# Performance work log

Measured on AMD Instinct MI355X. Metric: run time of the kernel, lower is better.

## Reference

```python
import jax, jax.numpy as jnp
import numpy as np

NC = 120000            # active coarse voxels
D, H, W = 16, 256, 256 # coarse grid
NF = 2 * NC            # active fine voxels (upsample output)
CIN, COUT = 128, 64


def _build_pairs():
    """Build spconv-style (in_idx, out_idx) pair maps per kernel offset.
    Padding: in_idx = NC (dummy zero feature row), out_idx = n_out (dropped row)."""
    rng = np.random.default_rng(0)
    flat = rng.choice(D * H * W, size=NC, replace=False)
    cz, cy, cx = np.unravel_index(flat, (D, H, W))
    lut = np.full(D * H * W, -1, np.int64)
    lut[flat] = np.arange(NC)

    def subm(offs):
        P = np.full((len(offs), NC, 2), NC, np.int32)
        for k, (dz, dy, dx) in enumerate(offs):
            nz, ny, nx = cz + dz, cy + dy, cx + dx
            ok = (nz >= 0) & (nz < D) & (ny >= 0) & (ny < H) & (nx >= 0) & (nx < W)
            nb = np.full(NC, -1, np.int64)
            nb[ok] = lut[(nz[ok] * H + ny[ok]) * W + nx[ok]]
            ok &= nb >= 0
            idx = np.nonzero(ok)[0]
            P[k, :len(idx), 0] = nb[idx]
            P[k, :len(idx), 1] = idx
        return P

    o33 = [(a, b, c) for a in (-1, 0, 1) for b in (-1, 0, 1) for c in (-1, 0, 1)]
    o13 = [(0, b, c) for b in (-1, 0, 1) for c in (-1, 0, 1)]   # kernel (1,3,3)
    o31 = [(a, 0, c) for a in (-1, 0, 1) for c in (-1, 0, 1)]   # kernel (3,1,3)

    # fine coords: each coarse voxel c spawns fine voxels 2c and 2c+1 (all dims)
    fz = np.concatenate([cz * 2, cz * 2 + 1])
    fy = np.concatenate([cy * 2, cy * 2 + 1])
    fx = np.concatenate([cx * 2, cx * 2 + 1])
    # inverse of a k=3, stride=2, pad=1 downsample: fine f <- coarse o where f = 2o - 1 + k
    Pu = np.zeros((27, NC, 2), np.int32)
    Pu[..., 0] = NC
    Pu[..., 1] = NF
    for k, (a, b, c) in enumerate([(a, b, c) for a in range(3) for b in range(3) for c in range(3)]):
        nz, ny, nx = fz + 1 - a, fy + 1 - b, fx + 1 - c
        ok = (nz % 2 == 0) & (ny % 2 == 0) & (nx % 2 == 0) & (nz >= 0) & (ny >= 0) & (nx >= 0)
        oz, oy, ox = nz // 2, ny // 2, nx // 2
        ok &= (oz < D) & (oy < H) & (ox < W)
        nb = np.full(NF, -1, np.int64)
        nb[ok] = lut[(oz[ok] * H + oy[ok]) * W + ox[ok]]
        ok &= nb >= 0
        idx = np.nonzero(ok)[0][:NC]
        Pu[k, :len(idx), 0] = nb[idx]
        Pu[k, :len(idx), 1] = idx
    return subm(o33), subm(o13), subm(o31), Pu


def setup_inputs():
    p33, p13, p31, pup = _build_pairs()
    ks = jax.random.split(jax.random.key(0), 12)
    f32 = jnp.float32
    return {
        "feats_x": jax.random.normal(ks[0], (NC, CIN), f32),
        "feats_skip": jax.random.normal(ks[1], (NC, CIN), f32),
        "W_trans": 0.05 * jax.random.normal(ks[2], (27, CIN, COUT), f32),
        "W1": 0.05 * jax.random.normal(ks[3], (9, COUT, COUT), f32),
        "W2": 0.05 * jax.random.normal(ks[4], (9, COUT, COUT), f32),
        "W_up": 0.05 * jax.random.normal(ks[5], (27, COUT, COUT), f32),
        "g0": 1.0 + 0.1 * jax.random.normal(ks[6], (COUT,), f32),
        "b0": 0.1 * jax.random.normal(ks[7], (COUT,), f32),
        "g1": 1.0 + 0.1 * jax.random.normal(ks[8], (COUT,), f32),
        "b1": 0.1 * jax.random.normal(ks[9], (COUT,), f32),
        "g2": 1.0 + 0.1 * jax.random.normal(ks[10], (COUT,), f32),
        "b2": 0.1 * jax.random.normal(ks[11], (COUT,), f32),
        "pairs33": jnp.asarray(p33),
        "pairs13": jnp.asarray(p13),
        "pairs31": jnp.asarray(p31),
        "pairs_up": jnp.asarray(pup),
    }


def _spconv(feats, Wk, pairs, n_out):
    # gather-GEMM-scatter sparse conv: feats [N,Cin], Wk [K,Cin,Cout], pairs [K,P,2]
    fp = jnp.concatenate([feats, jnp.zeros((1, feats.shape[1]), feats.dtype)], 0)
    out = jnp.zeros((n_out + 1, Wk.shape[2]), feats.dtype)
    for k in range(Wk.shape[0]):  # fixed small K (9 or 27)
        msg = fp[pairs[k, :, 0]] @ Wk[k]        # [P, Cout]
        out = out.at[pairs[k, :, 1]].add(msg)
    return out[:n_out]


def _bn(x, g, b):
    # BatchNorm1d (training-mode batch stats, eps=1e-5, biased var)
    m = x.mean(0)
    v = x.var(0)
    return (x - m) * jax.lax.rsqrt(v + 1e-5) * g + b


def reference(feats_x, feats_skip, W_trans, W1, W2, W_up,
              g0, b0, g1, b1, g2, b2,
              pairs33, pairs13, pairs31, pairs_up):
    x = feats_x + feats_skip                              # residual fuse with skip
    upA = _spconv(x, W_trans, pairs33, NC)                # trans_dilao (3x3x3 subm)
    upA = _bn(jax.nn.leaky_relu(upA, 0.01), g0, b0)       # act then BN (as in source)
    upE1 = _bn(_spconv(upA, W1, pairs13, NC), g1, b1)     # conv1x3 + bn1
    upE2 = _bn(_spconv(upA, W2, pairs31, NC), g2, b2)     # conv3x1 + bn2
    return _spconv(upE1 + upE2, W_up, pairs_up, NF)       # SparseInverseConv3d upsample
```

## Files before the change

### kernel.cpp

```cpp
#include <hip/hip_runtime.h>
#include <stdint.h>

typedef unsigned short u16;
typedef unsigned int u32;
typedef __bf16 bf16x8 __attribute__((ext_vector_type(8)));
typedef float floatx4 __attribute__((ext_vector_type(4)));

static constexpr int NC = 120000;
static constexpr int NF = 240000;

__device__ __forceinline__ float bf2f(u16 u) {
    union { u32 i; float f; } v; v.i = ((u32)u) << 16; return v.f;
}
__device__ __forceinline__ u16 f2bf(float f) {
    union { float f; u32 i; } v; v.f = f;
    u32 r = v.i + 0x7FFFu + ((v.i >> 16) & 1u);
    return (u16)(r >> 16);
}

__global__ void add_pad_k(const float* __restrict__ a, const float* __restrict__ b,
                          u16* __restrict__ xp) {
    int idx = blockIdx.x * blockDim.x + threadIdx.x;
    if (idx >= (NC + 1) * 32) return;
    uint2 vo;
    if (idx < NC * 32) {
        float4 va = ((const float4*)a)[idx];
        float4 vb = ((const float4*)b)[idx];
        vo.x = (u32)f2bf(va.x + vb.x) | ((u32)f2bf(va.y + vb.y) << 16);
        vo.y = (u32)f2bf(va.z + vb.z) | ((u32)f2bf(va.w + vb.w) << 16);
    } else {
        vo.x = vo.y = 0u;
    }
    ((uint2*)xp)[idx] = vo;
}

__global__ void transpose_w_k(const float* __restrict__ W, u16* __restrict__ Wt,
                              int K, int Cin) {
    int idx = blockIdx.x * blockDim.x + threadIdx.x;
    if (idx >= K * Cin * 64) return;
    int per = Cin * 64;
    int k = idx / per, rem = idx - k * per;
    int kc = rem >> 11;
    int r2 = rem & 2047;
    int nt = r2 >> 9, lane = (r2 >> 3) & 63, j = r2 & 7;
    int ci = kc * 32 + (lane >> 4) * 8 + j;
    int co = nt * 16 + (lane & 15);
    Wt[idx] = f2bf(W[(size_t)(k * Cin + ci) * 64 + co]);
}

__device__ __forceinline__ int upslot_to_k(int s) {
    if (s == 0) return 13;
    int e = s - 1;
    return 18 * ((e >> 2) & 1) + 6 * ((e >> 1) & 1) + 2 * (e & 1);
}
__global__ void transpose_wup_k(const float* __restrict__ W, u16* __restrict__ Wt) {
    int idx = blockIdx.x * blockDim.x + threadIdx.x;
    if (idx >= 9 * 4096) return;
    int s = idx >> 12, rem = idx & 4095;
    int kc = rem >> 11, r2 = rem & 2047;
    int nt = r2 >> 9, lane = (r2 >> 3) & 63, j = r2 & 7;
    int ci = kc * 32 + (lane >> 4) * 8 + j;
    int co = nt * 16 + (lane & 15);
    int k = upslot_to_k(s);
    Wt[idx] = f2bf(W[(size_t)(k * 64 + ci) * 64 + co]);
}

__global__ void fill_k(int* __restrict__ p, int n, int val) {
    int i = blockIdx.x * blockDim.x + threadIdx.x;
    if (i < n) p[i] = val;
}

__global__ void scatter_k(const int* __restrict__ pairs, int* __restrict__ inv,
                          int npairs, int n_out) {
    int i = blockIdx.x * blockDim.x + threadIdx.x;
    if (i >= npairs) return;
    int in = pairs[2 * i], out = pairs[2 * i + 1];
    if (out < n_out) inv[(i / NC) * n_out + out] = in;
}

__global__ void scatter_up_k(const int* __restrict__ pairs, int* __restrict__ inv) {
    int i = blockIdx.x * blockDim.x + threadIdx.x;
    if (i >= 27 * NC) return;
    int in = pairs[2 * i], out = pairs[2 * i + 1];
    if (out >= NF) return;
    int k = i / NC;
    int a = k / 9, r = k - a * 9, b = r / 3, c = r - b * 3;
    int s;
    if (k == 13) {
        s = 0;
    } else if (((a | b | c) & 1) == 0) {
        s = 1 + (a >> 1) * 4 + (b >> 1) * 2 + (c >> 1);
    } else {
        return;
    }
    inv[(size_t)s * NF + out] = in;
}

template <int TCIN, int KMAX, int R, bool F32OUT, int MINW>
__global__ __launch_bounds__(256, MINW) void spconv_k(
    const u16* __restrict__ feats,
    const int* __restrict__ invA, const u16* __restrict__ wTA, void* __restrict__ outA,
    const int* __restrict__ invB, const u16* __restrict__ wTB, void* __restrict__ outB,
    int nb0, int n_outA, int n_outB, int kliveA, int kliveB) {
    constexpr int KC = TCIN / 32;
    constexpr int WFRAGS = TCIN * 64 / 8;
    constexpr int NST = WFRAGS / 256;
    __shared__ bf16x8 wlds[2][WFRAGS];

    const int tid = threadIdx.x;
    const int wave = tid >> 6, lane = tid & 63;
    const int l15 = lane & 15, quad = lane >> 4;
    const bool second = (int)blockIdx.x >= nb0;
    const int bid = second ? (int)blockIdx.x - nb0 : (int)blockIdx.x;
    const int* __restrict__ inv = second ? invB : invA;
    const u16* __restrict__ wT  = second ? wTB : wTA;
    void* __restrict__ outv     = second ? outB : outA;
    const int n_out             = second ? n_outB : n_outA;
    const int Klive             = second ? kliveB : kliveA;

    const int blockrow = bid * (R * 64);
    const int base = blockrow + wave * 16 + l15;

    floatx4 acc[R][4];
#pragma unroll
    for (int t = 0; t < R; ++t)
#pragma unroll
        for (int nt = 0; nt < 4; ++nt) acc[t][nt] = (floatx4)(0.0f);

    int rc[R], rn[R];
#pragma unroll
    for (int t = 0; t < R; ++t) rc[t] = inv[base + t * 64];
#pragma unroll
    for (int t = 0; t < R; ++t) rn[t] = inv[n_out + base + t * 64];

    {
        const bf16x8* wsrc = (const bf16x8*)wT + tid;
#pragma unroll
        for (int s = 0; s < NST; ++s) wlds[0][tid + s * 256] = wsrc[s * 256];
    }

    bf16x8 abuf[2][R][KC];
#pragma unroll
    for (int t = 0; t < R; ++t) {
        if (__any(rc[t] != NC)) {
            const u16* ap = feats + (size_t)rc[t] * TCIN + quad * 8;
#pragma unroll
            for (int kc = 0; kc < KC; ++kc) abuf[0][t][kc] = *(const bf16x8*)(ap + kc * 32);
        }
    }
    __syncthreads();

#pragma unroll
    for (int k = 0; k < KMAX; ++k) {
        if (k < Klive) {
            const int cur = k & 1, nxt = cur ^ 1;
            if (k + 1 < Klive) {
                const bf16x8* wsrc = (const bf16x8*)(wT + (size_t)(k + 1) * (64 * TCIN)) + tid;
                bf16x8 st[NST];
#pragma unroll
                for (int s = 0; s < NST; ++s) st[s] = wsrc[s * 256];
#pragma unroll
                for (int s = 0; s < NST; ++s) wlds[nxt][tid + s * 256] = st[s];
            }
            int rf[R];
#pragma unroll
            for (int t = 0; t < R; ++t) rf[t] = NC;
            if (k + 2 < Klive) {
                const int* invf = inv + (size_t)(k + 2) * n_out;
#pragma unroll
                for (int t = 0; t < R; ++t) rf[t] = invf[base + t * 64];
            }
            bool lv[R], any = false;
#pragma unroll
            for (int t = 0; t < R; ++t) { lv[t] = __any(rc[t] != NC); any = any || lv[t]; }
            if (k + 1 < Klive) {
#pragma unroll
                for (int t = 0; t < R; ++t) {
                    if (__any(rn[t] != NC)) {
                        const u16* ap = feats + (size_t)rn[t] * TCIN + quad * 8;
#pragma unroll
                        for (int kc = 0; kc < KC; ++kc)
                            abuf[nxt][t][kc] = *(const bf16x8*)(ap + kc * 32);
                    }
                }
            }
            if (any) {
                bf16x8 b[KC][4];
#pragma unroll
                for (int kc = 0; kc < KC; ++kc)
#pragma unroll
                    for (int nt = 0; nt < 4; ++nt)
                        b[kc][nt] = wlds[cur][(kc * 4 + nt) * 64 + lane];
#pragma unroll
                for (int t = 0; t < R; ++t) {
                    if (lv[t]) {
#pragma unroll
                        for (int kc = 0; kc < KC; ++kc)
#pragma unroll
                            for (int nt = 0; nt < 4; ++nt)
                                acc[t][nt] = __builtin_amdgcn_mfma_f32_16x16x32_bf16(
                                    abuf[cur][t][kc], b[kc][nt], acc[t][nt], 0, 0, 0);
                    }
                }
            }
            __syncthreads();
#pragma unroll
            for (int t = 0; t < R; ++t) { rc[t] = rn[t]; rn[t] = rf[t]; }
        }
    }
#pragma unroll
    for (int t = 0; t < R; ++t) {
#pragma unroll
        for (int nt = 0; nt < 4; ++nt) {
#pragma unroll
            for (int r = 0; r < 4; ++r) {
                float v = acc[t][nt][r];
                int row = blockrow + t * 64 + wave * 16 + quad * 4 + r;
                size_t oi = (size_t)row * 64 + nt * 16 + l15;
                if (F32OUT) ((float*)outv)[oi] = v;
                else        ((u16*)outv)[oi] = f2bf(v);
            }
        }
    }
}

__global__ void stats2_k(const u16* __restrict__ ra, const u16* __restrict__ rb,
                         float* __restrict__ sa, float* __restrict__ sb, int half) {
    const u16* raw = ((int)blockIdx.x < half) ? ra : rb;
    float* sums    = ((int)blockIdx.x < half) ? sa : sb;
    int bx = ((int)blockIdx.x < half) ? (int)blockIdx.x : (int)blockIdx.x - half;
    int tid = threadIdx.x;
    int wave = tid >> 6, c = tid & 63;
    int gw = bx * 4 + wave;
    int GW = half * 4;
    float s = 0.f, q = 0.f;
    for (int r = gw; r < NC; r += GW) {
        float v = bf2f(raw[(size_t)r * 64 + c]);
        s += v; q += v * v;
    }
    __shared__ float sbm[4][64], qbm[4][64];
    sbm[wave][c] = s; qbm[wave][c] = q;
    __syncthreads();
    if (tid < 64) {
        float S = sbm[0][tid] + sbm[1][tid] + sbm[2][tid] + sbm[3][tid];
        float Q = qbm[0][tid] + qbm[1][tid] + qbm[2][tid] + qbm[3][tid];
        atomicAdd(&sums[tid], S);
        atomicAdd(&sums[64 + tid], Q);
    }
}

template <bool F32IN>
__global__ void stats_pair_k(const void* __restrict__ ra, const void* __restrict__ rb,
                             float* __restrict__ sums, int nblk) {
    int tid = threadIdx.x;
    int wave = tid >> 6, c = tid & 63;
    int gw = (int)blockIdx.x * 4 + wave;
    int GW = nblk * 4;
    float s = 0.f, q = 0.f;
    for (int r = gw; r < NC; r += GW) {
        size_t o = (size_t)r * 64 + c;
        float v = F32IN ? (((const float*)ra)[o] + ((const float*)rb)[o])
                        : (bf2f(((const u16*)ra)[o]) + bf2f(((const u16*)rb)[o]));
        v = v > 0.f ? v : 0.01f * v;
        s += v; q += v * v;
    }
    __shared__ float sbm[4][64], qbm[4][64];
    sbm[wave][c] = s; qbm[wave][c] = q;
    __syncthreads();
    if (tid < 64) {
        float S = sbm[0][tid] + sbm[1][tid] + sbm[2][tid] + sbm[3][tid];
        float Q = qbm[0][tid] + qbm[1][tid] + qbm[2][tid] + qbm[3][tid];
        atomicAdd(&sums[tid], S);
        atomicAdd(&sums[64 + tid], Q);
    }
}

__global__ void finalize_k(const float* __restrict__ sums, const float* __restrict__ g,
                           const float* __restrict__ bb, float* __restrict__ scsh) {
    int c = threadIdx.x;
    if (c < 64) {
        float m = sums[c] / (float)NC;
        float v = sums[64 + c] / (float)NC - m * m;
        float sc = g[c] * rsqrtf(v + 1e-5f);
        scsh[c] = sc;
        scsh[64 + c] = bb[c] - m * sc;
    }
}

template <bool F32IN>
__global__ void apply_pair_k(const void* __restrict__ ra, const void* __restrict__ rb,
                             const float* __restrict__ scsh, u16* __restrict__ up) {
    int idx = blockIdx.x * blockDim.x + threadIdx.x;
    if (idx >= (NC + 1) * 64) return;
    int c = idx & 63, i = idx >> 6;
    u16 o = 0;
    if (i < NC) {
        float v = F32IN ? (((const float*)ra)[idx] + ((const float*)rb)[idx])
                        : (bf2f(((const u16*)ra)[idx]) + bf2f(((const u16*)rb)[idx]));
        v = v > 0.f ? v : 0.01f * v;
        o = f2bf(v * scsh[c] + scsh[64 + c]);
    }
    up[idx] = o;
}

__global__ void apply12_k(const u16* __restrict__ rb, const u16* __restrict__ rc,
                          const float* __restrict__ s1, const float* __restrict__ s2,
                          u16* __restrict__ up) {
    int idx = blockIdx.x * blockDim.x + threadIdx.x;
    if (idx >= (NC + 1) * 64) return;
    int c = idx & 63, i = idx >> 6;
    float v = bf2f(rb[idx]) * s1[c] + s1[64 + c] + bf2f(rc[idx]) * s2[c] + s2[64 + c];
    up[idx] = (i < NC) ? f2bf(v) : (u16)0;
}

extern "C" void kernel_launch(void* const* d_in, const int* in_sizes, int n_in,
                              void* d_out, int out_size, void* d_ws, size_t ws_size,
                              hipStream_t stream) {
    const float* feats_x    = (const float*)d_in[0];
    const float* feats_skip = (const float*)d_in[1];
    const float* W_trans    = (const float*)d_in[2];
    const float* W1         = (const float*)d_in[3];
    const float* W2         = (const float*)d_in[4];
    const float* W_up       = (const float*)d_in[5];
    const float* g0 = (const float*)d_in[6],  *b0 = (const float*)d_in[7];
    const float* g1 = (const float*)d_in[8],  *b1 = (const float*)d_in[9];
    const float* g2 = (const float*)d_in[10], *b2 = (const float*)d_in[11];
    const int* pairs33 = (const int*)d_in[12];
    const int* pairs13 = (const int*)d_in[13];
    const int* pairs31 = (const int*)d_in[14];
    const int* pairs_up = (const int*)d_in[15];
    float* outp = (float*)d_out;

    const bool bigws = ws_size >= (size_t)130267392;

    char* ws = (char*)d_ws;
    size_t off = 0;
    auto alloc = [&](size_t bytes) {
        char* p = ws + off;
        off += (bytes + 255) & ~(size_t)255;
        return p;
    };
    u16* xp    = (u16*)alloc(30720256);
    int* inv33 = (int*)alloc(12960000);
    int* inv13 = (int*)alloc(4320000);
    int* inv31 = (int*)alloc(4320000);
    void* rawF0 = (void*)alloc(bigws ? 30720000 : 15360000);
    void* rawF1 = (void*)alloc(bigws ? 30720000 : 15360000);
    u16* upA   = (u16*)alloc(15360128);
    u16* WtA   = (u16*)alloc(27 * 128 * 64 * 2);
    u16* Wt1   = (u16*)alloc(9 * 64 * 64 * 2);
    u16* Wt2   = (u16*)alloc(9 * 64 * 64 * 2);
    u16* WtU   = (u16*)alloc(9 * 64 * 64 * 2);
    float* stats = (float*)alloc(6 * 128 * 4);
    int* inv_up = (int*)xp;
    u16* rawB = (u16*)rawF0;
    u16* rawC = (u16*)rawF1;
    u16* upE  = (u16*)inv33;
    float *sums0 = stats,        *sums1 = stats + 128, *sums2 = stats + 256;
    float *scsh0 = stats + 384,  *scsh1 = stats + 512, *scsh2 = stats + 640;

    const int B = 256;
    hipMemsetAsync(stats, 0, 6 * 128 * 4, stream);

    transpose_w_k<<<(27 * 128 * 64 + 255) / 256, B, 0, stream>>>(W_trans, WtA, 27, 128);
    transpose_w_k<<<(9 * 64 * 64 + 255) / 256, B, 0, stream>>>(W1, Wt1, 9, 64);
    transpose_w_k<<<(9 * 64 * 64 + 255) / 256, B, 0, stream>>>(W2, Wt2, 9, 64);
    transpose_wup_k<<<(9 * 64 * 64 + 255) / 256, B, 0, stream>>>(W_up, WtU);

    add_pad_k<<<((NC + 1) * 32 + 255) / 256, B, 0, stream>>>(feats_x, feats_skip, xp);

    fill_k<<<(45 * NC + 255) / 256, B, 0, stream>>>(inv33, 45 * NC, NC);
    scatter_k<<<(27 * NC + 255) / 256, B, 0, stream>>>(pairs33, inv33, 27 * NC, NC);
    scatter_k<<<(9 * NC + 255) / 256, B, 0, stream>>>(pairs13, inv13, 9 * NC, NC);
    scatter_k<<<(9 * NC + 255) / 256, B, 0, stream>>>(pairs31, inv31, 9 * NC, NC);

    if (bigws) {
        spconv_k<128, 14, 3, true, 2><<<1250, B, 0, stream>>>(
            xp, inv33, WtA, rawF0, inv33 + 14 * NC, WtA + 14 * 128 * 64, rawF1,
            625, NC, NC, 14, 13);
        stats_pair_k<true><<<240, B, 0, stream>>>(rawF0, rawF1, sums0, 240);
        finalize_k<<<1, 64, 0, stream>>>(sums0, g0, b0, scsh0);
        apply_pair_k<true><<<((NC + 1) * 64 + 255) / 256, B, 0, stream>>>(
            rawF0, rawF1, scsh0, upA);
    } else {
        spconv_k<128, 14, 3, false, 2><<<1250, B, 0, stream>>>(
            xp, inv33, WtA, rawF0, inv33 + 14 * NC, WtA + 14 * 128 * 64, rawF1,
            625, NC, NC, 14, 13);
        stats_pair_k<false><<<240, B, 0, stream>>>(rawF0, rawF1, sums0, 240);
        finalize_k<<<1, 64, 0, stream>>>(sums0, g0, b0, scsh0);
        apply_pair_k<false><<<((NC + 1) * 64 + 255) / 256, B, 0, stream>>>(
            rawF0, rawF1, scsh0, upA);
    }

    fill_k<<<(9 * NF + 255) / 256, B, 0, stream>>>(inv_up, 9 * NF, NC);
    scatter_up_k<<<(27 * NC + 255) / 256, B, 0, stream>>>(pairs_up, inv_up);

    spconv_k<64, 9, 3, false, 3><<<1250, B, 0, stream>>>(
        upA, inv13, Wt1, rawB, inv31, Wt2, rawC, 625, NC, NC, 9, 9);
    stats2_k<<<240, B, 0, stream>>>(rawB, rawC, sums1, sums2, 120);
    finalize_k<<<1, 64, 0, stream>>>(sums1, g1, b1, scsh1);
    finalize_k<<<1, 64, 0, stream>>>(sums2, g2, b2, scsh2);

    apply12_k<<<((NC + 1) * 64 + 255) / 256, B, 0, stream>>>(rawB, rawC, scsh1, scsh2, upE);

    spconv_k<64, 8, 3, true, 3><<<1250, B, 0, stream>>>(
        upE, inv_up, WtU, outp,
        inv_up + (size_t)NF + NC, WtU + 64 * 64, (void*)(outp + (size_t)NC * 64),
        625, NF, NF, 1, 8);
}
```

Measured before the change: 533.3 us.

## Run full 27-offset conv per block, fuse leaky-relu, add XCD block swizzle

The first 3x3x3 conv stops splitting the kernel offsets across two block groups whose partial sums were added later. Each block now accumulates all 27 offsets and applies leaky-relu in its epilogue, so the stats and apply passes read a single bf16 buffer. Rows per wave drop from 3 to 2, which changes grid sizes and needs bounds clamping on the ragged last block. Block IDs are remapped so neighbouring row ranges land on the same XCD. The first conv now has fewer blocks, each with a longer serial offset loop.

```diff
diff --git a/kernel.cpp b/kernel.cpp
--- a/kernel.cpp
+++ b/kernel.cpp
@@ -16,6 +16,12 @@
     union { float f; u32 i; } v; v.f = f;
     u32 r = v.i + 0x7FFFu + ((v.i >> 16) & 1u);
     return (u16)(r >> 16);
+}
+
+__device__ __forceinline__ int xcd_swz(int bid, int nb) {
+    int q = nb >> 3, r = nb & 7;
+    int x = bid & 7, i = bid >> 3;
+    return (x < r ? x * (q + 1) : r * (q + 1) + (x - r) * q) + i;
 }
 
 __global__ void add_pad_k(const float* __restrict__ a, const float* __restrict__ b,
@@ -96,12 +102,12 @@
     inv[(size_t)s * NF + out] = in;
 }
 
-template <int TCIN, int KMAX, int R, bool F32OUT, int MINW>
+template <int TCIN, int KMAX, int R, bool LEAKY, bool F32OUT, int MINW>
 __global__ __launch_bounds__(256, MINW) void spconv_k(
     const u16* __restrict__ feats,
     const int* __restrict__ invA, const u16* __restrict__ wTA, void* __restrict__ outA,
     const int* __restrict__ invB, const u16* __restrict__ wTB, void* __restrict__ outB,
-    int nb0, int n_outA, int n_outB, int kliveA, int kliveB) {
+    int nb0, int n_outA, int n_outB, int kliveA, int kliveB, int nrA, int nrB) {
     constexpr int KC = TCIN / 32;
     constexpr int WFRAGS = TCIN * 64 / 8;
     constexpr int NST = WFRAGS / 256;
@@ -111,16 +117,23 @@
     const int wave = tid >> 6, lane = tid & 63;
     const int l15 = lane & 15, quad = lane >> 4;
     const bool second = (int)blockIdx.x >= nb0;
-    const int bid = second ? (int)blockIdx.x - nb0 : (int)blockIdx.x;
+    int bid = second ? (int)blockIdx.x - nb0 : (int)blockIdx.x;
+    const int nb = second ? (int)gridDim.x - nb0 : nb0;
+    bid = xcd_swz(bid, nb);
     const int* __restrict__ inv = second ? invB : invA;
     const u16* __restrict__ wT  = second ? wTB : wTA;
     void* __restrict__ outv     = second ? outB : outA;
     const int n_out             = second ? n_outB : n_outA;
     const int Klive             = second ? kliveB : kliveA;
+    const int nr                = second ? nrB : nrA;
 
     const int blockrow = bid * (R * 64);
     const int base = blockrow + wave * 16 + l15;
 
+    int rowix[R];
+#pragma unroll
+    for (int t = 0; t < R; ++t) rowix[t] = min(base + t * 64, nr - 1);
+
     floatx4 acc[R][4];
 #pragma unroll
     for (int t = 0; t < R; ++t)
@@ -129,9 +142,9 @@
 
     int rc[R], rn[R];
 #pragma unroll
-    for (int t = 0; t < R; ++t) rc[t] = inv[base + t * 64];
-#pragma unroll
-    for (int t = 0; t < R; ++t) rn[t] = inv[n_out + base + t * 64];
+    for (int t = 0; t < R; ++t) rc[t] = inv[rowix[t]];
+#pragma unroll
+    for (int t = 0; t < R; ++t) rn[t] = inv[n_out + rowix[t]];
 
     {
         const bf16x8* wsrc = (const bf16x8*)wT + tid;
@@ -168,7 +181,7 @@
             if (k + 2 < Klive) {
                 const int* invf = inv + (size_t)(k + 2) * n_out;
 #pragma unroll
-                for (int t = 0; t < R; ++t) rf[t] = invf[base + t * 64];
+                for (int t = 0; t < R; ++t) rf[t] = invf[rowix[t]];
             }
             bool lv[R], any = false;
 #pragma unroll
@@ -215,12 +228,37 @@
 #pragma unroll
             for (int r = 0; r < 4; ++r) {
                 float v = acc[t][nt][r];
+                if (LEAKY) v = v > 0.f ? v : 0.01f * v;
                 int row = blockrow + t * 64 + wave * 16 + quad * 4 + r;
-                size_t oi = (size_t)row * 64 + nt * 16 + l15;
-                if (F32OUT) ((float*)outv)[oi] = v;
-                else        ((u16*)outv)[oi] = f2bf(v);
+                if (row < nr) {
+                    size_t oi = (size_t)row * 64 + nt * 16 + l15;
+                    if (F32OUT) ((float*)outv)[oi] = v;
+                    else        ((u16*)outv)[oi] = f2bf(v);
+                }
             }
         }
+    }
+}
+
+__global__ void stats1_k(const u16* __restrict__ raw, float* __restrict__ sums,
+                         int nblk) {
+    int tid = threadIdx.x;
+    int wave = tid >> 6, c = tid & 63;
+    int gw = (int)blockIdx.x * 4 + wave;
+    int GW = nblk * 4;
+    float s = 0.f, q = 0.f;
+    for (int r = gw; r < NC; r += GW) {
+        float v = bf2f(raw[(size_t)r * 64 + c]);
+        s += v; q += v * v;
+    }
+    __shared__ float sbm[4][64], qbm[4][64];
+    sbm[wave][c] = s; qbm[wave][c] = q;
+    __syncthreads();
+    if (tid < 64) {
+        float S = sbm[0][tid] + sbm[1][tid] + sbm[2][tid] + sbm[3][tid];
+        float Q = qbm[0][tid] + qbm[1][tid] + qbm[2][tid] + qbm[3][tid];
+        atomicAdd(&sums[tid], S);
+        atomicAdd(&sums[64 + tid], Q);
     }
 }
 
@@ -249,32 +287,6 @@
     }
 }
 
-template <bool F32IN>
-__global__ void stats_pair_k(const void* __restrict__ ra, const void* __restrict__ rb,
-                             float* __restrict__ sums, int nblk) {
-    int tid = threadIdx.x;
-    int wave = tid >> 6, c = tid & 63;
-    int gw = (int)blockIdx.x * 4 + wave;
-    int GW = nblk * 4;
-    float s = 0.f, q = 0.f;
-    for (int r = gw; r < NC; r += GW) {
-        size_t o = (size_t)r * 64 + c;
-        float v = F32IN ? (((const float*)ra)[o] + ((const float*)rb)[o])
-                        : (bf2f(((const u16*)ra)[o]) + bf2f(((const u16*)rb)[o]));
-        v = v > 0.f ? v : 0.01f * v;
-        s += v; q += v * v;
-    }
-    __shared__ float sbm[4][64], qbm[4][64];
-    sbm[wave][c] = s; qbm[wave][c] = q;
-    __syncthreads();
-    if (tid < 64) {
-        float S = sbm[0][tid] + sbm[1][tid] + sbm[2][tid] + sbm[3][tid];
-        float Q = qbm[0][tid] + qbm[1][tid] + qbm[2][tid] + qbm[3][tid];
-        atomicAdd(&sums[tid], S);
-        atomicAdd(&sums[64 + tid], Q);
-    }
-}
-
 __global__ void finalize_k(const float* __restrict__ sums, const float* __restrict__ g,
                            const float* __restrict__ bb, float* __restrict__ scsh) {
     int c = threadIdx.x;
@@ -287,20 +299,12 @@
     }
 }
 
-template <bool F32IN>
-__global__ void apply_pair_k(const void* __restrict__ ra, const void* __restrict__ rb,
-                             const float* __restrict__ scsh, u16* __restrict__ up) {
+__global__ void apply0_k(const u16* __restrict__ raw, const float* __restrict__ scsh,
+                         u16* __restrict__ up) {
     int idx = blockIdx.x * blockDim.x + threadIdx.x;
     if (idx >= (NC + 1) * 64) return;
     int c = idx & 63, i = idx >> 6;
-    u16 o = 0;
-    if (i < NC) {
-        float v = F32IN ? (((const float*)ra)[idx] + ((const float*)rb)[idx])
-                        : (bf2f(((const u16*)ra)[idx]) + bf2f(((const u16*)rb)[idx]));
-        v = v > 0.f ? v : 0.01f * v;
-        o = f2bf(v * scsh[c] + scsh[64 + c]);
-    }
-    up[idx] = o;
+    up[idx] = (i < NC) ? f2bf(bf2f(raw[idx]) * scsh[c] + scsh[64 + c]) : (u16)0;
 }
 
 __global__ void apply12_k(const u16* __restrict__ rb, const u16* __restrict__ rc,
@@ -331,8 +335,6 @@
     const int* pairs_up = (const int*)d_in[15];
     float* outp = (float*)d_out;
 
-    const bool bigws = ws_size >= (size_t)130267392;
-
     char* ws = (char*)d_ws;
     size_t off = 0;
     auto alloc = [&](size_t bytes) {
@@ -344,8 +346,8 @@
     int* inv33 = (int*)alloc(12960000);
     int* inv13 = (int*)alloc(4320000);
     int* inv31 = (int*)alloc(4320000);
-    void* rawF0 = (void*)alloc(bigws ? 30720000 : 15360000);
-    void* rawF1 = (void*)alloc(bigws ? 30720000 : 15360000);
+    u16* rawA  = (u16*)alloc(15360000);
+    u16* rawC  = (u16*)alloc(15360000);
     u16* upA   = (u16*)alloc(15360128);
     u16* WtA   = (u16*)alloc(27 * 128 * 64 * 2);
     u16* Wt1   = (u16*)alloc(9 * 64 * 64 * 2);
@@ -353,8 +355,7 @@
     u16* WtU   = (u16*)alloc(9 * 64 * 64 * 2);
     float* stats = (float*)alloc(6 * 128 * 4);
     int* inv_up = (int*)xp;
-    u16* rawB = (u16*)rawF0;
-    u16* rawC = (u16*)rawF1;
+    u16* rawB = rawA;
     u16* upE  = (u16*)inv33;
     float *sums0 = stats,        *sums1 = stats + 128, *sums2 = stats + 256;
     float *scsh0 = stats + 384,  *scsh1 = stats + 512, *scsh2 = stats + 640;
@@ -374,37 +375,25 @@
     scatter_k<<<(9 * NC + 255) / 256, B, 0, stream>>>(pairs13, inv13, 9 * NC, NC);
     scatter_k<<<(9 * NC + 255) / 256, B, 0, stream>>>(pairs31, inv31, 9 * NC, NC);
 
-    if (bigws) {
-        spconv_k<128, 14, 3, true, 2><<<1250, B, 0, stream>>>(
-            xp, inv33, WtA, rawF0, inv33 + 14 * NC, WtA + 14 * 128 * 64, rawF1,
-            625, NC, NC, 14, 13);
-        stats_pair_k<true><<<240, B, 0, stream>>>(rawF0, rawF1, sums0, 240);
-        finalize_k<<<1, 64, 0, stream>>>(sums0, g0, b0, scsh0);
-        apply_pair_k<true><<<((NC + 1) * 64 + 255) / 256, B, 0, stream>>>(
-            rawF0, rawF1, scsh0, upA);
-    } else {
-        spconv_k<128, 14, 3, false, 2><<<1250, B, 0, stream>>>(
-            xp, inv33, WtA, rawF0, inv33 + 14 * NC, WtA + 14 * 128 * 64, rawF1,
-            625, NC, NC, 14, 13);
-        stats_pair_k<false><<<240, B, 0, stream>>>(rawF0, rawF1, sums0, 240);
-        finalize_k<<<1, 64, 0, stream>>>(sums0, g0, b0, scsh0);
-        apply_pair_k<false><<<((NC + 1) * 64 + 255) / 256, B, 0, stream>>>(
-            rawF0, rawF1, scsh0, upA);
-    }
+    spconv_k<128, 27, 2, true, false, 2><<<938, B, 0, stream>>>(
+        xp, inv33, WtA, rawA, inv33, WtA, rawA, 938, NC, NC, 27, 27, NC, NC);
+    stats1_k<<<240, B, 0, stream>>>(rawA, sums0, 240);
+    finalize_k<<<1, 64, 0, stream>>>(sums0, g0, b0, scsh0);
+    apply0_k<<<((NC + 1) * 64 + 255) / 256, B, 0, stream>>>(rawA, scsh0, upA);
 
     fill_k<<<(9 * NF + 255) / 256, B, 0, stream>>>(inv_up, 9 * NF, NC);
     scatter_up_k<<<(27 * NC + 255) / 256, B, 0, stream>>>(pairs_up, inv_up);
 
-    spconv_k<64, 9, 3, false, 3><<<1250, B, 0, stream>>>(
-        upA, inv13, Wt1, rawB, inv31, Wt2, rawC, 625, NC, NC, 9, 9);
+    spconv_k<64, 9, 2, false, false, 3><<<1876, B, 0, stream>>>(
+        upA, inv13, Wt1, rawB, inv31, Wt2, rawC, 938, NC, NC, 9, 9, NC, NC);
     stats2_k<<<240, B, 0, stream>>>(rawB, rawC, sums1, sums2, 120);
     finalize_k<<<1, 64, 0, stream>>>(sums1, g1, b1, scsh1);
     finalize_k<<<1, 64, 0, stream>>>(sums2, g2, b2, scsh2);
 
     apply12_k<<<((NC + 1) * 64 + 255) / 256, B, 0, stream>>>(rawB, rawC, scsh1, scsh2, upE);
 
-    spconv_k<64, 8, 3, true, 3><<<1250, B, 0, stream>>>(
+    spconv_k<64, 8, 2, false, true, 3><<<1876, B, 0, stream>>>(
         upE, inv_up, WtU, outp,
         inv_up + (size_t)NF + NC, WtU + 64 * 64, (void*)(outp + (size_t)NC * 64),
-        625, NF, NF, 1, 8);
-}
+        938, NF, NF, 1, 8, NC, NC);
+}
```

Result: no change. 523.4 us (-1.8%).
